# Optimization experiments

Measured on AMD Instinct MI355X. Metric: run time of the kernel, lower is better.

## Reference

```python
import jax, jax.numpy as jnp
import numpy as np

D_MODEL = 1024
N_HEADS = 16
D_HEAD = D_MODEL // N_HEADS
B, S = 4, 2048


def setup_inputs() -> dict:
    key = jax.random.key(0)
    ks = jax.random.split(key, 8)
    scale = 1.0 / np.sqrt(D_MODEL)
    x = jax.random.normal(ks[0], (B, S, D_MODEL), dtype=jnp.float32)
    relative_bias = jax.random.normal(ks[1], (1, N_HEADS, S, S), dtype=jnp.float32)
    w_q = jax.random.normal(ks[2], (D_MODEL, D_MODEL), dtype=jnp.float32) * scale
    w_k = jax.random.normal(ks[3], (D_MODEL, D_MODEL), dtype=jnp.float32) * scale
    w_v = jax.random.normal(ks[4], (D_MODEL, D_MODEL), dtype=jnp.float32) * scale
    w_o = jax.random.normal(ks[5], (D_MODEL, D_MODEL), dtype=jnp.float32) * scale
    b_o = jax.random.normal(ks[6], (D_MODEL,), dtype=jnp.float32) * 0.02
    return {"x": x, "relative_bias": relative_bias, "w_q": w_q, "w_k": w_k,
            "w_v": w_v, "w_o": w_o, "b_o": b_o}


def reference(x, relative_bias, w_q, w_k, w_v, w_o, b_o):
    b, s, d = x.shape
    # torch nn.Linear computes x @ W^T; weights stored [out, in]
    def proj(w):
        y = jnp.einsum('bsd,ed->bse', x, w)  # [B,S,D]
        return y.reshape(b, s, N_HEADS, D_HEAD).transpose(0, 2, 1, 3)  # [B,H,S,Dh]
    q, k, v = proj(w_q), proj(w_k), proj(w_v)
    scores = jnp.einsum('bhqd,bhkd->bhqk', q, k) / jnp.sqrt(
        jnp.asarray(D_HEAD, x.dtype)) + relative_bias
    attn = jax.nn.softmax(scores, axis=-1)
    ctx = jnp.einsum('bhqk,bhkd->bhqd', attn, v)
    ctx = ctx.transpose(0, 2, 1, 3).reshape(b, s, d)
    return jnp.einsum('bsd,ed->bse', ctx, w_o) + b_o
```

## Files before the change

### kernel.cpp

```cpp
#include <hip/hip_runtime.h>
#include <hip/hip_bf16.h>

#define D_MODEL 1024
#define N_HEADS 16
#define D_HEAD  64
#define BATCH   4
#define SEQ     2048

typedef __attribute__((ext_vector_type(8))) short short8;
typedef __attribute__((ext_vector_type(8))) unsigned short ushort8;
typedef __attribute__((ext_vector_type(4))) unsigned short ushort4v;
typedef __attribute__((ext_vector_type(4))) float f32x4;

__device__ inline unsigned short f2bf(float f) {
  unsigned int u = __builtin_bit_cast(unsigned int, f);
  u += 0x7fffu + ((u >> 16) & 1u);
  return (unsigned short)(u >> 16);
}

__device__ inline f32x4 mfma_bf16(short8 a, short8 b, f32x4 c) {
  return __builtin_amdgcn_mfma_f32_16x16x32_bf16(a, b, c, 0, 0, 0);
}

__global__ void cvt_kernel(const float* __restrict__ src,
                           unsigned short* __restrict__ dst, int n) {
  int i = (blockIdx.x * 256 + threadIdx.x) * 8;
  if (i >= n) return;
  float4 a = *reinterpret_cast<const float4*>(src + i);
  float4 b = *reinterpret_cast<const float4*>(src + i + 4);
  ushort8 o;
  o[0] = f2bf(a.x); o[1] = f2bf(a.y); o[2] = f2bf(a.z); o[3] = f2bf(a.w);
  o[4] = f2bf(b.x); o[5] = f2bf(b.y); o[6] = f2bf(b.z); o[7] = f2bf(b.w);
  *reinterpret_cast<ushort8*>(dst + i) = o;
}

template<int NBYTES>
__device__ inline void stage_swz(const unsigned short* g0, int g_stride_elems,
                                 unsigned short* lds0, int tid) {
#pragma unroll
  for (int it = 0; it < NBYTES / 4096; ++it) {
    int o = it * 4096 + tid * 16;
    int r = o >> 7;
    int cb = (o & 127) ^ ((r & 7) << 4);
    unsigned short* g = const_cast<unsigned short*>(g0) +
                        (size_t)r * g_stride_elems + (cb >> 1);
    unsigned short* l = lds0 + (o >> 1);
    __builtin_amdgcn_global_load_lds((__attribute__((address_space(1))) void*)g,
                                     (__attribute__((address_space(3))) void*)l,
                                     16, 0, 0);
  }
}

__device__ inline short8 frag_ld(const unsigned short* tile, int row, int col_el) {
  int cb = (col_el << 1) ^ ((row & 7) << 4);
  return *reinterpret_cast<const short8*>(
      reinterpret_cast<const char*>(tile) + row * 128 + cb);
}

__launch_bounds__(256, 2)
__global__ void qkv_gemm(const unsigned short* __restrict__ xb,
                         const unsigned short* __restrict__ wb,
                         unsigned short* __restrict__ Qo,
                         unsigned short* __restrict__ Ko,
                         unsigned short* __restrict__ Vt) {
  __shared__ __align__(16) unsigned short As[128][64];
  __shared__ __align__(16) unsigned short Bs[128][64];
  const int z = blockIdx.z;
  const int m0 = blockIdx.y * 128;
  const int n0 = blockIdx.x * 128;
  const int tid = threadIdx.x;
  const int lane = tid & 63;
  const int wv = tid >> 6;
  const int wr = wv >> 1, wc = wv & 1;
  const int lrow = lane & 15;
  const int lk8 = (lane >> 4) << 3;
  const unsigned short* w = wb + (size_t)z * D_MODEL * D_MODEL;

  f32x4 acc[4][4];
  const f32x4 zero = {0.f, 0.f, 0.f, 0.f};
#pragma unroll
  for (int i = 0; i < 4; ++i)
#pragma unroll
    for (int j = 0; j < 4; ++j) acc[i][j] = zero;

  for (int k0 = 0; k0 < D_MODEL; k0 += 64) {
    __syncthreads();
    stage_swz<16384>(xb + (size_t)m0 * D_MODEL + k0, D_MODEL, &As[0][0], tid);
    stage_swz<16384>(w  + (size_t)n0 * D_MODEL + k0, D_MODEL, &Bs[0][0], tid);
    __syncthreads();
#pragma unroll
    for (int ks = 0; ks < 2; ++ks) {
      short8 af[4], bfr[4];
#pragma unroll
      for (int mi = 0; mi < 4; ++mi)
        af[mi] = frag_ld(&As[0][0], wr * 64 + mi * 16 + lrow, ks * 32 + lk8);
#pragma unroll
      for (int ni = 0; ni < 4; ++ni)
        bfr[ni] = frag_ld(&Bs[0][0], wc * 64 + ni * 16 + lrow, ks * 32 + lk8);
      if (z != 2) {
#pragma unroll
        for (int mi = 0; mi < 4; ++mi)
#pragma unroll
          for (int ni = 0; ni < 4; ++ni)
            acc[mi][ni] = mfma_bf16(af[mi], bfr[ni], acc[mi][ni]);
      } else {
#pragma unroll
        for (int ni = 0; ni < 4; ++ni)
#pragma unroll
          for (int mi = 0; mi < 4; ++mi)
            acc[ni][mi] = mfma_bf16(bfr[ni], af[mi], acc[ni][mi]);
      }
    }
  }

  const int lrr = (lane >> 4) << 2;
  if (z != 2) {
    unsigned short* dst = (z == 0) ? Qo : Ko;
    const float scale = (z == 0) ? 0.125f : 1.0f;
#pragma unroll
    for (int mi = 0; mi < 4; ++mi)
#pragma unroll
      for (int ni = 0; ni < 4; ++ni)
#pragma unroll
        for (int r = 0; r < 4; ++r) {
          int m = m0 + wr * 64 + mi * 16 + lrr + r;
          int e = n0 + wc * 64 + ni * 16 + lrow;
          int b = m >> 11, s = m & (SEQ - 1);
          int h = e >> 6, dh = e & 63;
          dst[((size_t)(b * N_HEADS + h) * SEQ + s) * D_HEAD + dh] =
              f2bf(acc[mi][ni][r] * scale);
        }
  } else {
#pragma unroll
    for (int ni = 0; ni < 4; ++ni)
#pragma unroll
      for (int mi = 0; mi < 4; ++mi)
#pragma unroll
        for (int r = 0; r < 4; ++r) {
          int e = n0 + wc * 64 + ni * 16 + lrr + r;
          int m = m0 + wr * 64 + mi * 16 + lrow;
          int b = m >> 11, s = m & (SEQ - 1);
          int h = e >> 6, dh = e & 63;
          Vt[((size_t)(b * N_HEADS + h) * D_HEAD + dh) * SEQ + s] =
              f2bf(acc[ni][mi][r]);
        }
  }
}

__launch_bounds__(256, 3)
__global__ void attn_kernel(const unsigned short* __restrict__ Q,
                            const unsigned short* __restrict__ K,
                            const unsigned short* __restrict__ Vt,
                            const float* __restrict__ bias,
                            unsigned short* __restrict__ ctx) {
  __shared__ __align__(16) unsigned short Qs[64][64];
  __shared__ __align__(16) unsigned short Ks[2][64][64];
  __shared__ __align__(16) unsigned short Vs[2][64][64];
  __shared__ __align__(16) unsigned short Ps[4][16][72];

  const int bh = blockIdx.y;
  const int b = bh >> 4, h = bh & (N_HEADS - 1);
  const int q0 = blockIdx.x * 64;
  const int tid = threadIdx.x, lane = tid & 63, wv = tid >> 6;
  const int lrow = lane & 15;
  const int lgrp = lane >> 4;
  const int lk8 = lgrp << 3;
  const int lrr = lgrp << 2;

  const size_t qk_base = (size_t)bh * SEQ * D_HEAD;
  const unsigned short* Vbase = Vt + (size_t)bh * D_HEAD * SEQ;

  stage_swz<8192>(Q + qk_base + (size_t)q0 * D_HEAD, D_HEAD, &Qs[0][0], tid);
  stage_swz<8192>(K + qk_base, D_HEAD, &Ks[0][0][0], tid);
  stage_swz<8192>(Vbase, SEQ, &Vs[0][0][0], tid);

  const float* bp = bias + (size_t)h * SEQ * SEQ +
                    (size_t)(q0 + wv * 16 + lrow) * SEQ + lrr;
  float4 bcur[4], bnext[4];
#pragma unroll
  for (int nt = 0; nt < 4; ++nt)
    bcur[nt] = *reinterpret_cast<const float4*>(bp + nt * 16);

  __syncthreads();

  short8 qf[2];
#pragma unroll
  for (int ks = 0; ks < 2; ++ks)
    qf[ks] = frag_ld(&Qs[0][0], wv * 16 + lrow, ks * 32 + lk8);

  float m_run = -1e30f, l_run = 0.f;
  f32x4 o_acc[4];
  const f32x4 zero = {0.f, 0.f, 0.f, 0.f};
#pragma unroll
  for (int dt = 0; dt < 4; ++dt) o_acc[dt] = zero;

  for (int kt = 0; kt < 32; ++kt) {
    const int cur = kt & 1;
    if (kt < 31) {
      const int kvn = (kt + 1) * 64;
      stage_swz<8192>(K + qk_base + (size_t)kvn * D_HEAD, D_HEAD,
                      &Ks[cur ^ 1][0][0], tid);
      stage_swz<8192>(Vbase + kvn, SEQ, &Vs[cur ^ 1][0][0], tid);
#pragma unroll
      for (int nt = 0; nt < 4; ++nt)
        bnext[nt] = *reinterpret_cast<const float4*>(bp + kvn + nt * 16);
    }

    f32x4 s[4];
#pragma unroll
    for (int nt = 0; nt < 4; ++nt) s[nt] = zero;
    __builtin_amdgcn_s_setprio(1);
#pragma unroll
    for (int ks = 0; ks < 2; ++ks)
#pragma unroll
      for (int nt = 0; nt < 4; ++nt) {
        short8 kf = frag_ld(&Ks[cur][0][0], nt * 16 + lrow, ks * 32 + lk8);
        s[nt] = mfma_bf16(kf, qf[ks], s[nt]);
      }
    __builtin_amdgcn_s_setprio(0);

    float p[4][4];
    float pmax = -1e30f;
#pragma unroll
    for (int nt = 0; nt < 4; ++nt)
#pragma unroll
      for (int r = 0; r < 4; ++r) {
        float v = s[nt][r] + ((const float*)&bcur[nt])[r];
        p[nt][r] = v;
        pmax = fmaxf(pmax, v);
      }
    pmax = fmaxf(pmax, __shfl_xor(pmax, 16));
    pmax = fmaxf(pmax, __shfl_xor(pmax, 32));
    float mnew = fmaxf(m_run, pmax);
    float corr = __expf(m_run - mnew);
    float rs = 0.f;
#pragma unroll
    for (int nt = 0; nt < 4; ++nt)
#pragma unroll
      for (int r = 0; r < 4; ++r) {
        float e = __expf(p[nt][r] - mnew);
        p[nt][r] = e;
        rs += e;
      }
    rs += __shfl_xor(rs, 16);
    rs += __shfl_xor(rs, 32);
    l_run = l_run * corr + rs;
    m_run = mnew;

#pragma unroll
    for (int nt = 0; nt < 4; ++nt) {
      ushort4v pk;
#pragma unroll
      for (int r = 0; r < 4; ++r) pk[r] = f2bf(p[nt][r]);
      *reinterpret_cast<ushort4v*>(&Ps[wv][lrow][nt * 16 + lrr]) = pk;
    }

#pragma unroll
    for (int r = 0; r < 4; ++r) {
      float c = __shfl(corr, lrr + r);
#pragma unroll
      for (int dt = 0; dt < 4; ++dt) o_acc[dt][r] *= c;
    }

    short8 pf[2];
#pragma unroll
    for (int ks = 0; ks < 2; ++ks)
      pf[ks] = *reinterpret_cast<const short8*>(&Ps[wv][lrow][ks * 32 + lk8]);
    __builtin_amdgcn_s_setprio(1);
#pragma unroll
    for (int ks = 0; ks < 2; ++ks)
#pragma unroll
      for (int dt = 0; dt < 4; ++dt) {
        short8 vf = frag_ld(&Vs[cur][0][0], dt * 16 + lrow, ks * 32 + lk8);
        o_acc[dt] = mfma_bf16(pf[ks], vf, o_acc[dt]);
      }
    __builtin_amdgcn_s_setprio(0);

    __syncthreads();
    if (kt < 31) {
#pragma unroll
      for (int nt = 0; nt < 4; ++nt) bcur[nt] = bnext[nt];
    }
  }

  float inv = 1.0f / l_run;
#pragma unroll
  for (int r = 0; r < 4; ++r) {
    float invq = __shfl(inv, lrr + r);
    int qs = q0 + wv * 16 + lrr + r;
#pragma unroll
    for (int dt = 0; dt < 4; ++dt)
      ctx[((size_t)(b * SEQ) + qs) * D_MODEL + h * 64 + dt * 16 + lrow] =
          f2bf(o_acc[dt][r] * invq);
  }
}

__launch_bounds__(256, 2)
__global__ void out_gemm(const unsigned short* __restrict__ cb,
                         const unsigned short* __restrict__ wo,
                         const float* __restrict__ bo,
                         float* __restrict__ out) {
  __shared__ __align__(16) unsigned short As[128][64];
  __shared__ __align__(16) unsigned short Bs[128][64];
  const int m0 = blockIdx.y * 128;
  const int n0 = blockIdx.x * 128;
  const int tid = threadIdx.x;
  const int lane = tid & 63;
  const int wv = tid >> 6;
  const int wr = wv >> 1, wc = wv & 1;
  const int lrow = lane & 15;
  const int lk8 = (lane >> 4) << 3;

  f32x4 acc[4][4];
  const f32x4 zero = {0.f, 0.f, 0.f, 0.f};
#pragma unroll
  for (int i = 0; i < 4; ++i)
#pragma unroll
    for (int j = 0; j < 4; ++j) acc[i][j] = zero;

  for (int k0 = 0; k0 < D_MODEL; k0 += 64) {
    __syncthreads();
    stage_swz<16384>(cb + (size_t)m0 * D_MODEL + k0, D_MODEL, &As[0][0], tid);
    stage_swz<16384>(wo + (size_t)n0 * D_MODEL + k0, D_MODEL, &Bs[0][0], tid);
    __syncthreads();
#pragma unroll
    for (int ks = 0; ks < 2; ++ks) {
      short8 af[4], bfr[4];
#pragma unroll
      for (int mi = 0; mi < 4; ++mi)
        af[mi] = frag_ld(&As[0][0], wr * 64 + mi * 16 + lrow, ks * 32 + lk8);
#pragma unroll
      for (int ni = 0; ni < 4; ++ni)
        bfr[ni] = frag_ld(&Bs[0][0], wc * 64 + ni * 16 + lrow, ks * 32 + lk8);
#pragma unroll
      for (int mi = 0; mi < 4; ++mi)
#pragma unroll
        for (int ni = 0; ni < 4; ++ni)
          acc[mi][ni] = mfma_bf16(af[mi], bfr[ni], acc[mi][ni]);
    }
  }

  const int lrr = (lane >> 4) << 2;
#pragma unroll
  for (int mi = 0; mi < 4; ++mi)
#pragma unroll
    for (int ni = 0; ni < 4; ++ni)
#pragma unroll
      for (int r = 0; r < 4; ++r) {
        int m = m0 + wr * 64 + mi * 16 + lrr + r;
        int e = n0 + wc * 64 + ni * 16 + lrow;
        out[(size_t)m * D_MODEL + e] = acc[mi][ni][r] + bo[e];
      }
}

extern "C" void kernel_launch(void* const* d_in, const int* in_sizes, int n_in,
                              void* d_out, int out_size, void* d_ws, size_t ws_size,
                              hipStream_t stream) {
  const float* x    = (const float*)d_in[0];
  const float* bias = (const float*)d_in[1];
  const float* w_q  = (const float*)d_in[2];
  const float* w_k  = (const float*)d_in[3];
  const float* w_v  = (const float*)d_in[4];
  const float* w_o  = (const float*)d_in[5];
  const float* b_o  = (const float*)d_in[6];
  float* out = (float*)d_out;

  const size_t NX = (size_t)BATCH * SEQ * D_MODEL;
  const size_t NW = (size_t)D_MODEL * D_MODEL;

  unsigned short* xb    = (unsigned short*)d_ws;
  unsigned short* wqkvb = xb + NX;
  unsigned short* wob   = wqkvb + 3 * NW;
  unsigned short* Qb    = wob + NW;
  unsigned short* Kb    = Qb + NX;
  unsigned short* Vtb   = Kb + NX;
  unsigned short* ctxb  = Vtb + NX;

  cvt_kernel<<<(int)(NX / 2048), 256, 0, stream>>>(x, xb, (int)NX);
  cvt_kernel<<<(int)(NW / 2048), 256, 0, stream>>>(w_q, wqkvb, (int)NW);
  cvt_kernel<<<(int)(NW / 2048), 256, 0, stream>>>(w_k, wqkvb + NW, (int)NW);
  cvt_kernel<<<(int)(NW / 2048), 256, 0, stream>>>(w_v, wqkvb + 2 * NW, (int)NW);
  cvt_kernel<<<(int)(NW / 2048), 256, 0, stream>>>(w_o, wob, (int)NW);

  qkv_gemm<<<dim3(8, 64, 3), 256, 0, stream>>>(xb, wqkvb, Qb, Kb, Vtb);
  attn_kernel<<<dim3(32, 64), 256, 0, stream>>>(Qb, Kb, Vtb, bias, ctxb);
  out_gemm<<<dim3(8, 64), 256, 0, stream>>>(ctxb, wob, b_o, out);
}
```

Before: 356.0 us.

## Process all four batches per attention block to reuse relative-bias loads

Each attention block now handles one (head, query tile) for all four batch elements, so every relative-bias tile is read from global memory once instead of once per batch. K/V tiles for successive batches are double-buffered in an interleaved order, and the bias loads are marked nontemporal. The cost is four sets of accumulators and Q fragments per thread, which lowers the occupancy target from three to two, and a quarter as many blocks in the grid. Block IDs are also remapped so heads are interleaved across the grid.

```diff
diff --git a/kernel.cpp b/kernel.cpp
--- a/kernel.cpp
+++ b/kernel.cpp
@@ -147,7 +147,7 @@
   }
 }
 
-__launch_bounds__(256, 3)
+__launch_bounds__(256, 2)
 __global__ void attn_kernel(const unsigned short* __restrict__ Q,
                             const unsigned short* __restrict__ K,
                             const unsigned short* __restrict__ Vt,
@@ -158,140 +158,166 @@
   __shared__ __align__(16) unsigned short Vs[2][64][64];
   __shared__ __align__(16) unsigned short Ps[4][16][72];
 
-  const int bh = blockIdx.y;
-  const int b = bh >> 4, h = bh & (N_HEADS - 1);
-  const int q0 = blockIdx.x * 64;
+  const int fid = blockIdx.y * 32 + blockIdx.x;
+  const int j = fid >> 3;
+  const int h = (fid & 7) + 8 * (j & 1);
+  const int q0 = (j >> 1) * 64;
+
   const int tid = threadIdx.x, lane = tid & 63, wv = tid >> 6;
   const int lrow = lane & 15;
   const int lgrp = lane >> 4;
   const int lk8 = lgrp << 3;
   const int lrr = lgrp << 2;
 
-  const size_t qk_base = (size_t)bh * SEQ * D_HEAD;
-  const unsigned short* Vbase = Vt + (size_t)bh * D_HEAD * SEQ;
-
-  stage_swz<8192>(Q + qk_base + (size_t)q0 * D_HEAD, D_HEAD, &Qs[0][0], tid);
-  stage_swz<8192>(K + qk_base, D_HEAD, &Ks[0][0][0], tid);
-  stage_swz<8192>(Vbase, SEQ, &Vs[0][0][0], tid);
+  short8 qf[4][2];
+#pragma unroll
+  for (int b = 0; b < 4; ++b) {
+    stage_swz<8192>(Q + ((size_t)(b * N_HEADS + h) * SEQ + q0) * D_HEAD,
+                    D_HEAD, &Qs[0][0], tid);
+    __syncthreads();
+#pragma unroll
+    for (int ks = 0; ks < 2; ++ks)
+      qf[b][ks] = frag_ld(&Qs[0][0], wv * 16 + lrow, ks * 32 + lk8);
+    __syncthreads();
+  }
+
+  stage_swz<8192>(K + (size_t)h * SEQ * D_HEAD, D_HEAD, &Ks[0][0][0], tid);
+  stage_swz<8192>(Vt + (size_t)h * D_HEAD * SEQ, SEQ, &Vs[0][0][0], tid);
 
   const float* bp = bias + (size_t)h * SEQ * SEQ +
                     (size_t)(q0 + wv * 16 + lrow) * SEQ + lrr;
-  float4 bcur[4], bnext[4];
+  f32x4 bcur[4], bnext[4];
 #pragma unroll
   for (int nt = 0; nt < 4; ++nt)
-    bcur[nt] = *reinterpret_cast<const float4*>(bp + nt * 16);
+    bcur[nt] = __builtin_nontemporal_load(
+        reinterpret_cast<const f32x4*>(bp + nt * 16));
+
+  float m_run[4], l_run[4];
+  f32x4 o_acc[4][4];
+  const f32x4 zero = {0.f, 0.f, 0.f, 0.f};
+#pragma unroll
+  for (int b = 0; b < 4; ++b) {
+    m_run[b] = -1e30f; l_run[b] = 0.f;
+#pragma unroll
+    for (int dt = 0; dt < 4; ++dt) o_acc[b][dt] = zero;
+  }
 
   __syncthreads();
 
-  short8 qf[2];
-#pragma unroll
-  for (int ks = 0; ks < 2; ++ks)
-    qf[ks] = frag_ld(&Qs[0][0], wv * 16 + lrow, ks * 32 + lk8);
-
-  float m_run = -1e30f, l_run = 0.f;
-  f32x4 o_acc[4];
-  const f32x4 zero = {0.f, 0.f, 0.f, 0.f};
-#pragma unroll
-  for (int dt = 0; dt < 4; ++dt) o_acc[dt] = zero;
-
   for (int kt = 0; kt < 32; ++kt) {
-    const int cur = kt & 1;
     if (kt < 31) {
-      const int kvn = (kt + 1) * 64;
-      stage_swz<8192>(K + qk_base + (size_t)kvn * D_HEAD, D_HEAD,
-                      &Ks[cur ^ 1][0][0], tid);
-      stage_swz<8192>(Vbase + kvn, SEQ, &Vs[cur ^ 1][0][0], tid);
 #pragma unroll
       for (int nt = 0; nt < 4; ++nt)
-        bnext[nt] = *reinterpret_cast<const float4*>(bp + kvn + nt * 16);
-    }
-
-    f32x4 s[4];
-#pragma unroll
-    for (int nt = 0; nt < 4; ++nt) s[nt] = zero;
-    __builtin_amdgcn_s_setprio(1);
-#pragma unroll
-    for (int ks = 0; ks < 2; ++ks)
+        bnext[nt] = __builtin_nontemporal_load(
+            reinterpret_cast<const f32x4*>(bp + (kt + 1) * 64 + nt * 16));
+    }
+
+#pragma unroll
+    for (int b = 0; b < 4; ++b) {
+      const int cur = b & 1;
+
+      if (!(kt == 31 && b == 3)) {
+        const int nb = (b + 1) & 3;
+        const int nkt = kt + (b == 3 ? 1 : 0);
+        stage_swz<8192>(K + (size_t)(nb * N_HEADS + h) * SEQ * D_HEAD +
+                            (size_t)nkt * 64 * D_HEAD,
+                        D_HEAD, &Ks[cur ^ 1][0][0], tid);
+        stage_swz<8192>(Vt + (size_t)(nb * N_HEADS + h) * D_HEAD * SEQ +
+                            nkt * 64,
+                        SEQ, &Vs[cur ^ 1][0][0], tid);
+      }
+
+      f32x4 s[4];
+#pragma unroll
+      for (int nt = 0; nt < 4; ++nt) s[nt] = zero;
+      __builtin_amdgcn_s_setprio(1);
+#pragma unroll
+      for (int ks = 0; ks < 2; ++ks)
+#pragma unroll
+        for (int nt = 0; nt < 4; ++nt) {
+          short8 kf = frag_ld(&Ks[cur][0][0], nt * 16 + lrow, ks * 32 + lk8);
+          s[nt] = mfma_bf16(kf, qf[b][ks], s[nt]);
+        }
+      __builtin_amdgcn_s_setprio(0);
+
+      float p[4][4];
+      float pmax = -1e30f;
+#pragma unroll
+      for (int nt = 0; nt < 4; ++nt)
+#pragma unroll
+        for (int r = 0; r < 4; ++r) {
+          float v = s[nt][r] + bcur[nt][r];
+          p[nt][r] = v;
+          pmax = fmaxf(pmax, v);
+        }
+      pmax = fmaxf(pmax, __shfl_xor(pmax, 16));
+      pmax = fmaxf(pmax, __shfl_xor(pmax, 32));
+      float mnew = fmaxf(m_run[b], pmax);
+      float corr = __expf(m_run[b] - mnew);
+      float rs = 0.f;
+#pragma unroll
+      for (int nt = 0; nt < 4; ++nt)
+#pragma unroll
+        for (int r = 0; r < 4; ++r) {
+          float e = __expf(p[nt][r] - mnew);
+          p[nt][r] = e;
+          rs += e;
+        }
+      rs += __shfl_xor(rs, 16);
+      rs += __shfl_xor(rs, 32);
+      l_run[b] = l_run[b] * corr + rs;
+      m_run[b] = mnew;
+
 #pragma unroll
       for (int nt = 0; nt < 4; ++nt) {
-        short8 kf = frag_ld(&Ks[cur][0][0], nt * 16 + lrow, ks * 32 + lk8);
-        s[nt] = mfma_bf16(kf, qf[ks], s[nt]);
+        ushort4v pk;
+#pragma unroll
+        for (int r = 0; r < 4; ++r) pk[r] = f2bf(p[nt][r]);
+        *reinterpret_cast<ushort4v*>(&Ps[wv][lrow][nt * 16 + lrr]) = pk;
       }
-    __builtin_amdgcn_s_setprio(0);
-
-    float p[4][4];
-    float pmax = -1e30f;
-#pragma unroll
-    for (int nt = 0; nt < 4; ++nt)
+
 #pragma unroll
       for (int r = 0; r < 4; ++r) {
-        float v = s[nt][r] + ((const float*)&bcur[nt])[r];
-        p[nt][r] = v;
-        pmax = fmaxf(pmax, v);
+        float c = __shfl(corr, lrr + r);
+#pragma unroll
+        for (int dt = 0; dt < 4; ++dt) o_acc[b][dt][r] *= c;
       }
-    pmax = fmaxf(pmax, __shfl_xor(pmax, 16));
-    pmax = fmaxf(pmax, __shfl_xor(pmax, 32));
-    float mnew = fmaxf(m_run, pmax);
-    float corr = __expf(m_run - mnew);
-    float rs = 0.f;
-#pragma unroll
-    for (int nt = 0; nt < 4; ++nt)
-#pragma unroll
-      for (int r = 0; r < 4; ++r) {
-        float e = __expf(p[nt][r] - mnew);
-        p[nt][r] = e;
-        rs += e;
-      }
-    rs += __shfl_xor(rs, 16);
-    rs += __shfl_xor(rs, 32);
-    l_run = l_run * corr + rs;
-    m_run = mnew;
-
-#pragma unroll
-    for (int nt = 0; nt < 4; ++nt) {
-      ushort4v pk;
-#pragma unroll
-      for (int r = 0; r < 4; ++r) pk[r] = f2bf(p[nt][r]);
-      *reinterpret_cast<ushort4v*>(&Ps[wv][lrow][nt * 16 + lrr]) = pk;
-    }
-
+
+      short8 pf[2];
+#pragma unroll
+      for (int ks = 0; ks < 2; ++ks)
+        pf[ks] = *reinterpret_cast<const short8*>(&Ps[wv][lrow][ks * 32 + lk8]);
+      __builtin_amdgcn_s_setprio(1);
+#pragma unroll
+      for (int ks = 0; ks < 2; ++ks)
+#pragma unroll
+        for (int dt = 0; dt < 4; ++dt) {
+          short8 vf = frag_ld(&Vs[cur][0][0], dt * 16 + lrow, ks * 32 + lk8);
+          o_acc[b][dt] = mfma_bf16(pf[ks], vf, o_acc[b][dt]);
+        }
+      __builtin_amdgcn_s_setprio(0);
+
+      __syncthreads();
+    }
+
+    if (kt < 31) {
+#pragma unroll
+      for (int nt = 0; nt < 4; ++nt) bcur[nt] = bnext[nt];
+    }
+  }
+
+#pragma unroll
+  for (int b = 0; b < 4; ++b) {
+    float inv = 1.0f / l_run[b];
 #pragma unroll
     for (int r = 0; r < 4; ++r) {
-      float c = __shfl(corr, lrr + r);
-#pragma unroll
-      for (int dt = 0; dt < 4; ++dt) o_acc[dt][r] *= c;
-    }
-
-    short8 pf[2];
-#pragma unroll
-    for (int ks = 0; ks < 2; ++ks)
-      pf[ks] = *reinterpret_cast<const short8*>(&Ps[wv][lrow][ks * 32 + lk8]);
-    __builtin_amdgcn_s_setprio(1);
-#pragma unroll
-    for (int ks = 0; ks < 2; ++ks)
-#pragma unroll
-      for (int dt = 0; dt < 4; ++dt) {
-        short8 vf = frag_ld(&Vs[cur][0][0], dt * 16 + lrow, ks * 32 + lk8);
-        o_acc[dt] = mfma_bf16(pf[ks], vf, o_acc[dt]);
-      }
-    __builtin_amdgcn_s_setprio(0);
-
-    __syncthreads();
-    if (kt < 31) {
-#pragma unroll
-      for (int nt = 0; nt < 4; ++nt) bcur[nt] = bnext[nt];
-    }
-  }
-
-  float inv = 1.0f / l_run;
-#pragma unroll
-  for (int r = 0; r < 4; ++r) {
-    float invq = __shfl(inv, lrr + r);
-    int qs = q0 + wv * 16 + lrr + r;
-#pragma unroll
-    for (int dt = 0; dt < 4; ++dt)
-      ctx[((size_t)(b * SEQ) + qs) * D_MODEL + h * 64 + dt * 16 + lrow] =
-          f2bf(o_acc[dt][r] * invq);
+      float invq = __shfl(inv, lrr + r);
+      int qs = q0 + wv * 16 + lrr + r;
+#pragma unroll
+      for (int dt = 0; dt < 4; ++dt)
+        ctx[((size_t)b * SEQ + qs) * D_MODEL + h * 64 + dt * 16 + lrow] =
+            f2bf(o_acc[b][dt][r] * invq);
+    }
   }
 }
 
@@ -383,6 +409,6 @@
   cvt_kernel<<<(int)(NW / 2048), 256, 0, stream>>>(w_o, wob, (int)NW);
 
   qkv_gemm<<<dim3(8, 64, 3), 256, 0, stream>>>(xb, wqkvb, Qb, Kb, Vtb);
-  attn_kernel<<<dim3(32, 64), 256, 0, stream>>>(Qb, Kb, Vtb, bias, ctxb);
+  attn_kernel<<<dim3(32, 16), 256, 0, stream>>>(Qb, Kb, Vtb, bias, ctxb);
   out_gemm<<<dim3(8, 64), 256, 0, stream>>>(ctxb, wob, b_o, out);
 }
```

Result: faster. 305.1 us (-14.3%).

## Remap attention blocks across XCDs, lazy softmax rescale, fold bias into MFMA

Applied to the files above, without the earlier changes.

Attention blocks are remapped so that the four batches sharing a head's relative bias tile run on the same XCD, which should improve L2 reuse of the large bias tensor. The Q staging buffer is dropped by loading Q through the K buffer, which frees LDS. The bias now initializes the score accumulator. Softmax uses exp2 with a folded log2e FMA, and the running max and output rescale are updated only when some row's max grows by more than a threshold, which skips most correction work but allows larger unnormalized exponent values.

```diff
diff --git a/kernel.cpp b/kernel.cpp
--- a/kernel.cpp
+++ b/kernel.cpp
@@ -6,6 +6,7 @@
 #define D_HEAD  64
 #define BATCH   4
 #define SEQ     2048
+#define LOG2E   1.44269504088896f
 
 typedef __attribute__((ext_vector_type(8))) short short8;
 typedef __attribute__((ext_vector_type(8))) unsigned short ushort8;
@@ -16,6 +17,10 @@
   unsigned int u = __builtin_bit_cast(unsigned int, f);
   u += 0x7fffu + ((u >> 16) & 1u);
   return (unsigned short)(u >> 16);
+}
+
+__device__ inline float exp2_fast(float x) {
+  return __builtin_amdgcn_exp2f(x);
 }
 
 __device__ inline f32x4 mfma_bf16(short8 a, short8 b, f32x4 c) {
@@ -153,40 +158,42 @@
                             const unsigned short* __restrict__ Vt,
                             const float* __restrict__ bias,
                             unsigned short* __restrict__ ctx) {
-  __shared__ __align__(16) unsigned short Qs[64][64];
   __shared__ __align__(16) unsigned short Ks[2][64][64];
   __shared__ __align__(16) unsigned short Vs[2][64][64];
   __shared__ __align__(16) unsigned short Ps[4][16][72];
 
-  const int bh = blockIdx.y;
-  const int b = bh >> 4, h = bh & (N_HEADS - 1);
-  const int q0 = blockIdx.x * 64;
+  const int lid = blockIdx.x + 32 * blockIdx.y + 512 * blockIdx.z;
+  const int xcd = lid & 7;
+  const int b   = (lid >> 3) & 3;
+  const int idx = xcd + ((lid >> 5) << 3);
+  const int h   = idx & 15;
+  const int q0  = (idx >> 4) << 6;
+
   const int tid = threadIdx.x, lane = tid & 63, wv = tid >> 6;
   const int lrow = lane & 15;
   const int lgrp = lane >> 4;
   const int lk8 = lgrp << 3;
   const int lrr = lgrp << 2;
 
-  const size_t qk_base = (size_t)bh * SEQ * D_HEAD;
-  const unsigned short* Vbase = Vt + (size_t)bh * D_HEAD * SEQ;
-
-  stage_swz<8192>(Q + qk_base + (size_t)q0 * D_HEAD, D_HEAD, &Qs[0][0], tid);
-  stage_swz<8192>(K + qk_base, D_HEAD, &Ks[0][0][0], tid);
-  stage_swz<8192>(Vbase, SEQ, &Vs[0][0][0], tid);
+  const size_t kvb = (size_t)(b * N_HEADS + h);
+
+  stage_swz<8192>(Q + (kvb * SEQ + q0) * D_HEAD, D_HEAD, &Ks[0][0][0], tid);
+  __syncthreads();
+  short8 qf[2];
+#pragma unroll
+  for (int ks = 0; ks < 2; ++ks)
+    qf[ks] = frag_ld(&Ks[0][0][0], wv * 16 + lrow, ks * 32 + lk8);
+  __syncthreads();
+
+  stage_swz<8192>(K + kvb * SEQ * D_HEAD, D_HEAD, &Ks[0][0][0], tid);
+  stage_swz<8192>(Vt + kvb * D_HEAD * SEQ, SEQ, &Vs[0][0][0], tid);
 
   const float* bp = bias + (size_t)h * SEQ * SEQ +
                     (size_t)(q0 + wv * 16 + lrow) * SEQ + lrr;
-  float4 bcur[4], bnext[4];
+  f32x4 bcur[4], bnext[4];
 #pragma unroll
   for (int nt = 0; nt < 4; ++nt)
-    bcur[nt] = *reinterpret_cast<const float4*>(bp + nt * 16);
-
-  __syncthreads();
-
-  short8 qf[2];
-#pragma unroll
-  for (int ks = 0; ks < 2; ++ks)
-    qf[ks] = frag_ld(&Qs[0][0], wv * 16 + lrow, ks * 32 + lk8);
+    bcur[nt] = *reinterpret_cast<const f32x4*>(bp + nt * 16);
 
   float m_run = -1e30f, l_run = 0.f;
   f32x4 o_acc[4];
@@ -194,21 +201,24 @@
 #pragma unroll
   for (int dt = 0; dt < 4; ++dt) o_acc[dt] = zero;
 
+  __syncthreads();
+
   for (int kt = 0; kt < 32; ++kt) {
     const int cur = kt & 1;
     if (kt < 31) {
-      const int kvn = (kt + 1) * 64;
-      stage_swz<8192>(K + qk_base + (size_t)kvn * D_HEAD, D_HEAD,
-                      &Ks[cur ^ 1][0][0], tid);
-      stage_swz<8192>(Vbase + kvn, SEQ, &Vs[cur ^ 1][0][0], tid);
+      stage_swz<8192>(K + kvb * SEQ * D_HEAD + (size_t)(kt + 1) * 64 * D_HEAD,
+                      D_HEAD, &Ks[cur ^ 1][0][0], tid);
+      stage_swz<8192>(Vt + kvb * D_HEAD * SEQ + (kt + 1) * 64, SEQ,
+                      &Vs[cur ^ 1][0][0], tid);
 #pragma unroll
       for (int nt = 0; nt < 4; ++nt)
-        bnext[nt] = *reinterpret_cast<const float4*>(bp + kvn + nt * 16);
+        bnext[nt] = *reinterpret_cast<const f32x4*>(bp + (kt + 1) * 64 +
+                                                    nt * 16);
     }
 
     f32x4 s[4];
 #pragma unroll
-    for (int nt = 0; nt < 4; ++nt) s[nt] = zero;
+    for (int nt = 0; nt < 4; ++nt) s[nt] = bcur[nt];
     __builtin_amdgcn_s_setprio(1);
 #pragma unroll
     for (int ks = 0; ks < 2; ++ks)
@@ -219,48 +229,48 @@
       }
     __builtin_amdgcn_s_setprio(0);
 
-    float p[4][4];
-    float pmax = -1e30f;
-#pragma unroll
-    for (int nt = 0; nt < 4; ++nt)
-#pragma unroll
-      for (int r = 0; r < 4; ++r) {
-        float v = s[nt][r] + ((const float*)&bcur[nt])[r];
-        p[nt][r] = v;
-        pmax = fmaxf(pmax, v);
-      }
+    float pmax =
+        fmaxf(fmaxf(fmaxf(fmaxf(s[0][0], s[0][1]), s[0][2]),
+                    fmaxf(fmaxf(s[1][0], s[1][1]), s[1][2])),
+              fmaxf(fmaxf(fmaxf(s[2][0], s[2][1]), s[2][2]),
+                    fmaxf(fmaxf(fmaxf(s[3][0], s[3][1]), s[3][2]),
+                          fmaxf(fmaxf(s[0][3], s[1][3]),
+                                fmaxf(s[2][3], s[3][3])))));
     pmax = fmaxf(pmax, __shfl_xor(pmax, 16));
     pmax = fmaxf(pmax, __shfl_xor(pmax, 32));
-    float mnew = fmaxf(m_run, pmax);
-    float corr = __expf(m_run - mnew);
+
+    if (!__all(pmax - m_run <= 7.6f)) {
+      float mnew = fmaxf(m_run, pmax);
+      float corr = exp2_fast((m_run - mnew) * LOG2E);
+      l_run *= corr;
+      m_run = mnew;
+#pragma unroll
+      for (int r = 0; r < 4; ++r) {
+        float c = __shfl(corr, lrr + r);
+#pragma unroll
+        for (int dt = 0; dt < 4; ++dt) o_acc[dt][r] *= c;
+      }
+    }
+
+    const float mL = m_run * LOG2E;
     float rs = 0.f;
 #pragma unroll
-    for (int nt = 0; nt < 4; ++nt)
-#pragma unroll
-      for (int r = 0; r < 4; ++r) {
-        float e = __expf(p[nt][r] - mnew);
-        p[nt][r] = e;
-        rs += e;
-      }
+    for (int nt = 0; nt < 4; ++nt) {
+      float p0 = exp2_fast(__builtin_fmaf(s[nt][0], LOG2E, -mL));
+      float p1 = exp2_fast(__builtin_fmaf(s[nt][1], LOG2E, -mL));
+      float p2 = exp2_fast(__builtin_fmaf(s[nt][2], LOG2E, -mL));
+      float p3 = exp2_fast(__builtin_fmaf(s[nt][3], LOG2E, -mL));
+      rs += (p0 + p1) + (p2 + p3);
+      ushort4v pk;
+      pk[0] = __builtin_bit_cast(unsigned short, __float2bfloat16(p0));
+      pk[1] = __builtin_bit_cast(unsigned short, __float2bfloat16(p1));
+      pk[2] = __builtin_bit_cast(unsigned short, __float2bfloat16(p2));
+      pk[3] = __builtin_bit_cast(unsigned short, __float2bfloat16(p3));
+      *reinterpret_cast<ushort4v*>(&Ps[wv][lrow][nt * 16 + lrr]) = pk;
+    }
     rs += __shfl_xor(rs, 16);
     rs += __shfl_xor(rs, 32);
-    l_run = l_run * corr + rs;
-    m_run = mnew;
-
-#pragma unroll
-    for (int nt = 0; nt < 4; ++nt) {
-      ushort4v pk;
-#pragma unroll
-      for (int r = 0; r < 4; ++r) pk[r] = f2bf(p[nt][r]);
-      *reinterpret_cast<ushort4v*>(&Ps[wv][lrow][nt * 16 + lrr]) = pk;
-    }
-
-#pragma unroll
-    for (int r = 0; r < 4; ++r) {
-      float c = __shfl(corr, lrr + r);
-#pragma unroll
-      for (int dt = 0; dt < 4; ++dt) o_acc[dt][r] *= c;
-    }
+    l_run += rs;
 
     short8 pf[2];
 #pragma unroll
@@ -290,7 +300,7 @@
     int qs = q0 + wv * 16 + lrr + r;
 #pragma unroll
     for (int dt = 0; dt < 4; ++dt)
-      ctx[((size_t)(b * SEQ) + qs) * D_MODEL + h * 64 + dt * 16 + lrow] =
+      ctx[((size_t)b * SEQ + qs) * D_MODEL + h * 64 + dt * 16 + lrow] =
           f2bf(o_acc[dt][r] * invq);
   }
 }
@@ -383,6 +393,6 @@
   cvt_kernel<<<(int)(NW / 2048), 256, 0, stream>>>(w_o, wob, (int)NW);
 
   qkv_gemm<<<dim3(8, 64, 3), 256, 0, stream>>>(xb, wqkvb, Qb, Kb, Vtb);
-  attn_kernel<<<dim3(32, 64), 256, 0, stream>>>(Qb, Kb, Vtb, bias, ctxb);
+  attn_kernel<<<dim3(32, 16, 4), 256, 0, stream>>>(Qb, Kb, Vtb, bias, ctxb);
   out_gemm<<<dim3(8, 64), 256, 0, stream>>>(ctxb, wob, b_o, out);
 }
```

New measurement: 328.4 us. 1.08x faster.
